# Kernel optimization log

Hardware: AMD Instinct MI355X
Metric: run time of the kernel (lower is better)

The kernel has to match this reference:

```python
import jax, jax.numpy as jnp
import numpy as np

NUM_USERS = 1_000_000
EMBED_DIM = 64
N_NODES = 16384
K = 50
NEG_INF = -1e30


def setup_inputs() -> dict:
    key = jax.random.key(0)
    ks = jax.random.split(key, 7)
    d = EMBED_DIM
    table = jax.random.normal(ks[0], (NUM_USERS, d), jnp.float32) * 0.02
    nodes = jax.random.randint(ks[1], (N_NODES,), 0, NUM_USERS)
    neigh_idx = jax.random.randint(ks[2], (N_NODES, K), 0, NUM_USERS)
    neigh_mask = jax.random.randint(ks[3], (N_NODES, K), 0, 2).astype(bool)
    neigh_mask = neigh_mask.at[:, 0].set(True)  # every node has >=1 neighbor
    W1 = jax.random.normal(ks[4], (2 * d, d), jnp.float32) / np.sqrt(2 * d)
    b1 = jnp.zeros((d,), jnp.float32)
    W2 = jax.random.normal(ks[5], (d, d), jnp.float32) / np.sqrt(d)
    b2 = jnp.zeros((d,), jnp.float32)
    W3 = jax.random.normal(ks[6], (d, 1), jnp.float32) / np.sqrt(d)
    b3 = jnp.zeros((1,), jnp.float32)
    return dict(table=table, W1=W1, b1=b1, W2=W2, b2=b2, W3=W3, b3=b3,
                nodes=nodes, neigh_idx=neigh_idx, neigh_mask=neigh_mask)


def reference(table, W1, b1, W2, b2, W3, b3, nodes, neigh_idx, neigh_mask):
    # Gather neighbor embeddings and center-node embeddings (eval mode: dropout off).
    E = table[neigh_idx]                                   # [N, K, d]
    U = table[nodes]                                       # [N, d]
    Uk = jnp.broadcast_to(U[:, None, :], E.shape)          # [N, K, d]
    x = jnp.concatenate([E, Uk], axis=-1)                  # [N, K, 2d]
    h = jax.nn.relu(x @ W1 + b1)                           # [N, K, d]
    h = jax.nn.relu(h @ W2 + b2)                           # [N, K, d]
    s = (h @ W3 + b3)[..., 0]                              # [N, K]
    # Masked softmax over the ragged neighbor dimension.
    s = jnp.where(neigh_mask, s, NEG_INF)
    att = jax.nn.softmax(s, axis=-1)                       # [N, K]
    # Attention-weighted sum of neighbor embeddings: e_u.T @ att_w per node.
    out = jnp.einsum('nk,nkd->nd', att, E)                 # [N, d]
    return out
```

## Files before the change

### kernel.cpp

```cpp
#include <hip/hip_runtime.h>
#include <hip/hip_bf16.h>

#define NN 16384
#define KK 50
#define DD 64

typedef __attribute__((ext_vector_type(8))) short bf16x8;
typedef __attribute__((ext_vector_type(4))) float f32x4;

__device__ __forceinline__ float bf2f(unsigned short u) {
    union { unsigned int i; float f; } v;
    v.i = ((unsigned int)u) << 16;
    return v.f;
}
__device__ __forceinline__ unsigned short f2bf(float f) {
    union { float f; unsigned int i; } v; v.f = f;
    unsigned int lsb = (v.i >> 16) & 1u;
    v.i += 0x7fffu + lsb;
    return (unsigned short)(v.i >> 16);
}
__device__ __forceinline__ unsigned int pk2bf(float lo, float hi) {
    unsigned int w;
    asm("v_cvt_pk_bf16_f32 %0, %1, %2" : "=v"(w) : "v"(lo), "v"(hi));
    return w;
}

template<int BF16>
__device__ __forceinline__ float ldv(const void* p, size_t i) {
    if (BF16) return bf2f(((const unsigned short*)p)[i]);
    else      return ((const float*)p)[i];
}

template<int BF16>
__device__ __forceinline__ f32x4 ld4(const void* p, size_t i) {
    if (BF16) {
        const ushort4 u = *(const ushort4*)((const unsigned short*)p + i);
        return (f32x4){bf2f(u.x), bf2f(u.y), bf2f(u.z), bf2f(u.w)};
    } else {
        return *(const f32x4*)((const float*)p + i);
    }
}

template<int BF16>
__device__ __forceinline__ bf16x8 load8(const void* p, size_t off) {
    if (BF16) {
        return *(const bf16x8*)((const unsigned short*)p + off);
    } else {
        const float* f = (const float*)p + off;
        const f32x4 a = *(const f32x4*)f;
        const f32x4 b = *(const f32x4*)(f + 4);
        union { bf16x8 v; unsigned int w[4]; } r;
        r.w[0] = pk2bf(a[0], a[1]);
        r.w[1] = pk2bf(a[2], a[3]);
        r.w[2] = pk2bf(b[0], b[1]);
        r.w[3] = pk2bf(b[2], b[3]);
        return r.v;
    }
}

__global__ void prep_kernel(const unsigned int* __restrict__ tw,
                            const unsigned int* __restrict__ mw,
                            const void* __restrict__ W1_,
                            const void* __restrict__ W2_,
                            int* __restrict__ flags,
                            unsigned short* __restrict__ W1top,
                            unsigned short* __restrict__ W1bot,
                            unsigned short* __restrict__ W2p) {
    __shared__ int sflags[2];
    const int t = threadIdx.x;
    if (t < 64) {
        const unsigned int w  = tw[t];
        const unsigned int lo = w & 0xFFFFu;
        const unsigned int ex = (lo >> 7) & 0xFFu;
        const bool bf_like = (ex >= 96u && ex <= 126u);
        const unsigned long long bb = __ballot(bf_like);
        bool found = false;
#pragma unroll
        for (int i = 0; i < 8; ++i) found |= (mw[t + i * 64] > 1u);
        const unsigned long long mb = __ballot(found);
        if (t == 0) {
            sflags[0] = (mb != 0ull) ? 1 : 0;
            sflags[1] = (__popcll(bb) >= 48) ? 1 : 0;
            flags[0] = sflags[0];
            flags[1] = sflags[1];
        }
    }
    __syncthreads();
    const int bf = sflags[1];
    {
        const int f = t >> 6, lane = t & 63;
        const int kt = f >> 2, nt = f & 3;
        const int q = lane >> 4, col = lane & 15;
#pragma unroll
        for (int j = 0; j < 8; ++j) {
            const int k = kt * 32 + q * 8 + j;
            const int n = nt * 16 + col;
            const float v = bf ? bf2f(((const unsigned short*)W1_)[k * 64 + n])
                               : ((const float*)W1_)[k * 64 + n];
            unsigned short* dst = (kt < 2) ? W1top : W1bot;
            const int fl = ((kt & 1) * 4 + nt);
            dst[((size_t)fl * 64 + lane) * 8 + j] = f2bf(v);
        }
    }
    if (t < 512) {
        const int f = t >> 6, lane = t & 63;
        const int kt = f >> 2, nt = f & 3;
        const int q = lane >> 4, col = lane & 15;
#pragma unroll
        for (int j = 0; j < 8; ++j) {
            const int k = kt * 32 + q * 8 + j;
            const int n = nt * 16 + col;
            const float v = bf ? bf2f(((const unsigned short*)W2_)[k * 64 + n])
                               : ((const float*)W2_)[k * 64 + n];
            W2p[((size_t)f * 64 + lane) * 8 + j] = f2bf(v);
        }
    }
}

template<int BF16>
__device__ __forceinline__ void uw_impl(
    const void* __restrict__ table_, const void* __restrict__ b1_,
    const int* __restrict__ nodes,
    const unsigned short* __restrict__ W1bot,
    float* __restrict__ UW)
{
    const int wave = threadIdx.x >> 6;
    const int lane = threadIdx.x & 63;
    const int q    = lane >> 4;
    const int col  = lane & 15;
    const int base = (blockIdx.x * 4 + wave) * 64;

    bf16x8 afrag[4][2];
#pragma unroll
    for (int mt = 0; mt < 4; ++mt) {
        const size_t row = (size_t)nodes[base + mt * 16 + col];
#pragma unroll
        for (int kt = 0; kt < 2; ++kt)
            afrag[mt][kt] = load8<BF16>(table_, row * 64 + kt * 32 + q * 8);
    }

    f32x4 acc[4][4];
#pragma unroll
    for (int mt = 0; mt < 4; ++mt)
#pragma unroll
        for (int nt = 0; nt < 4; ++nt) acc[mt][nt] = (f32x4){0.f, 0.f, 0.f, 0.f};

#pragma unroll
    for (int kt = 0; kt < 2; ++kt)
#pragma unroll
        for (int nt = 0; nt < 4; ++nt) {
            const bf16x8 b = *(const bf16x8*)(W1bot + ((size_t)(kt * 4 + nt) * 64 + lane) * 8);
#pragma unroll
            for (int mt = 0; mt < 4; ++mt)
                acc[mt][nt] = __builtin_amdgcn_mfma_f32_16x16x32_bf16(afrag[mt][kt], b, acc[mt][nt], 0, 0, 0);
        }

    float b1v[4];
#pragma unroll
    for (int nt = 0; nt < 4; ++nt) b1v[nt] = ldv<BF16>(b1_, nt * 16 + col);
#pragma unroll
    for (int mt = 0; mt < 4; ++mt)
#pragma unroll
        for (int nt = 0; nt < 4; ++nt)
#pragma unroll
            for (int r = 0; r < 4; ++r)
                UW[(size_t)(base + mt * 16 + q * 4 + r) * 64 + nt * 16 + col] =
                    acc[mt][nt][r] + b1v[nt];
}

__global__ __launch_bounds__(256) void uw_kernel(
    const void* __restrict__ table_, const void* __restrict__ b1_,
    const int* __restrict__ nodes, const int* __restrict__ flags,
    const unsigned short* __restrict__ W1bot, float* __restrict__ UW)
{
    if (flags[1]) uw_impl<1>(table_, b1_, nodes, W1bot, UW);
    else          uw_impl<0>(table_, b1_, nodes, W1bot, UW);
}

template<int BF16>
__device__ __forceinline__ void agg_impl(
    const void* __restrict__ table_,
    const void* __restrict__ b2_, const void* __restrict__ W3_,
    const int*  __restrict__ neigh_idx,
    const void* __restrict__ neigh_mask,
    int mu8,
    const unsigned short* __restrict__ W1top,
    const unsigned short* __restrict__ W2p,
    const float* __restrict__ UW,
    unsigned short* __restrict__ h1,
    float* __restrict__ scr,
    void* __restrict__ out_)
{
    const int lane = threadIdx.x & 63;
    const int n    = blockIdx.x * 2 + (threadIdx.x >> 6);
    const int q    = lane >> 4;
    const int col  = lane & 15;

    int  rowidx [4];
    bool rowmask[4];
#pragma unroll
    for (int mt = 0; mt < 4; ++mt) {
        const int k  = mt * 16 + col;
        const int kc = (k < KK) ? k : (KK - 1);
        const int ir = neigh_idx[(size_t)n * KK + kc];
        bool mk = mu8 ? (((const unsigned char*)neigh_mask)[(size_t)n * KK + kc] != 0)
                      : (((const int*)neigh_mask)[(size_t)n * KK + kc] != 0);
        mk = mk && (k < KK);
        rowmask[mt] = mk;
        rowidx[mt]  = mk ? ir : 0;
    }

    bf16x8 afrag[4][2];
#pragma unroll
    for (int mt = 0; mt < 4; ++mt)
#pragma unroll
        for (int kt = 0; kt < 2; ++kt)
            afrag[mt][kt] = load8<BF16>(table_, (size_t)rowidx[mt] * 64 + kt * 32 + q * 8);

#pragma unroll
    for (int ct = 0; ct < 4; ++ct) {
        const bf16x8 wA0 = *(const bf16x8*)(W1top + ((size_t)(0 * 4 + ct) * 64 + lane) * 8);
        const bf16x8 wA1 = *(const bf16x8*)(W1top + ((size_t)(1 * 4 + ct) * 64 + lane) * 8);
        f32x4 acc[4];
#pragma unroll
        for (int mt = 0; mt < 4; ++mt) acc[mt] = (f32x4){0.f, 0.f, 0.f, 0.f};
#pragma unroll
        for (int mt = 0; mt < 4; ++mt)
            acc[mt] = __builtin_amdgcn_mfma_f32_16x16x32_bf16(wA0, afrag[mt][0], acc[mt], 0, 0, 0);
#pragma unroll
        for (int mt = 0; mt < 4; ++mt)
            acc[mt] = __builtin_amdgcn_mfma_f32_16x16x32_bf16(wA1, afrag[mt][1], acc[mt], 0, 0, 0);

        const f32x4 uw4 = *(const f32x4*)&UW[(size_t)n * 64 + ct * 16 + q * 4];
#pragma unroll
        for (int mt = 0; mt < 4; ++mt) {
            const float h0 = fmaxf(acc[mt][0] + uw4[0], 0.f);
            const float hv1 = fmaxf(acc[mt][1] + uw4[1], 0.f);
            const float h2 = fmaxf(acc[mt][2] + uw4[2], 0.f);
            const float h3 = fmaxf(acc[mt][3] + uw4[3], 0.f);
            uint2 w;
            w.x = pk2bf(h0, hv1);
            w.y = pk2bf(h2, h3);
            *(uint2*)&h1[(size_t)(mt * 16 + col) * 72 + ct * 16 + q * 4] = w;
        }
    }
    __builtin_amdgcn_wave_barrier();

    bf16x8 bfrag[4][2];
#pragma unroll
    for (int mt = 0; mt < 4; ++mt)
#pragma unroll
        for (int kt = 0; kt < 2; ++kt)
            bfrag[mt][kt] = *(const bf16x8*)&h1[(size_t)(mt * 16 + col) * 72 + kt * 32 + q * 8];

    float p[4] = {0.f, 0.f, 0.f, 0.f};
#pragma unroll
    for (int ct = 0; ct < 4; ++ct) {
        const bf16x8 wB0 = *(const bf16x8*)(W2p + ((size_t)(0 * 4 + ct) * 64 + lane) * 8);
        const bf16x8 wB1 = *(const bf16x8*)(W2p + ((size_t)(1 * 4 + ct) * 64 + lane) * 8);
        f32x4 acc[4];
#pragma unroll
        for (int mt = 0; mt < 4; ++mt) acc[mt] = (f32x4){0.f, 0.f, 0.f, 0.f};
#pragma unroll
        for (int mt = 0; mt < 4; ++mt)
            acc[mt] = __builtin_amdgcn_mfma_f32_16x16x32_bf16(wB0, bfrag[mt][0], acc[mt], 0, 0, 0);
#pragma unroll
        for (int mt = 0; mt < 4; ++mt)
            acc[mt] = __builtin_amdgcn_mfma_f32_16x16x32_bf16(wB1, bfrag[mt][1], acc[mt], 0, 0, 0);

        const f32x4 b2v = ld4<BF16>(b2_, ct * 16 + q * 4);
        const f32x4 w3v = ld4<BF16>(W3_, ct * 16 + q * 4);
#pragma unroll
        for (int mt = 0; mt < 4; ++mt) {
            float t = 0.f;
#pragma unroll
            for (int r = 0; r < 4; ++r)
                t += fmaxf(acc[mt][r] + b2v[r], 0.f) * w3v[r];
            p[mt] += t;
        }
    }

#pragma unroll
    for (int mt = 0; mt < 4; ++mt) {
        p[mt] += __shfl_xor(p[mt], 16, 64);
        p[mt] += __shfl_xor(p[mt], 32, 64);
        if (!rowmask[mt]) p[mt] = -1.0e30f;
    }

    float mx = fmaxf(fmaxf(p[0], p[1]), fmaxf(p[2], p[3]));
    mx = fmaxf(mx, __shfl_xor(mx, 1, 64));
    mx = fmaxf(mx, __shfl_xor(mx, 2, 64));
    mx = fmaxf(mx, __shfl_xor(mx, 4, 64));
    mx = fmaxf(mx, __shfl_xor(mx, 8, 64));

    float e[4], ls = 0.f;
#pragma unroll
    for (int mt = 0; mt < 4; ++mt) { e[mt] = __expf(p[mt] - mx); ls += e[mt]; }
    ls += __shfl_xor(ls, 1, 64);
    ls += __shfl_xor(ls, 2, 64);
    ls += __shfl_xor(ls, 4, 64);
    ls += __shfl_xor(ls, 8, 64);
    const float inv = 1.f / ls;

    float att[4];
#pragma unroll
    for (int mt = 0; mt < 4; ++mt) att[mt] = e[mt] * inv;

    float v[2][8];
#pragma unroll
    for (int kt = 0; kt < 2; ++kt)
#pragma unroll
        for (int j = 0; j < 8; ++j) v[kt][j] = 0.f;
#pragma unroll
    for (int mt = 0; mt < 4; ++mt)
#pragma unroll
        for (int kt = 0; kt < 2; ++kt)
#pragma unroll
            for (int j = 0; j < 8; ++j)
                v[kt][j] += att[mt] * bf2f(((const unsigned short*)&afrag[mt][kt])[j]);

#pragma unroll
    for (int off = 1; off <= 8; off <<= 1)
#pragma unroll
        for (int kt = 0; kt < 2; ++kt)
#pragma unroll
            for (int j = 0; j < 8; ++j)
                v[kt][j] += __shfl_xor(v[kt][j], off, 64);

    if (col == 0) {
#pragma unroll
        for (int kt = 0; kt < 2; ++kt) {
            *(f32x4*)&scr[kt * 32 + q * 8]     = (f32x4){v[kt][0], v[kt][1], v[kt][2], v[kt][3]};
            *(f32x4*)&scr[kt * 32 + q * 8 + 4] = (f32x4){v[kt][4], v[kt][5], v[kt][6], v[kt][7]};
        }
    }
    __builtin_amdgcn_wave_barrier();

    const float res = scr[lane];
    if (BF16) ((unsigned short*)out_)[(size_t)n * 64 + lane] = f2bf(res);
    else      ((float*)out_)[(size_t)n * 64 + lane] = res;
}

__global__ __launch_bounds__(128, 4) void agg_kernel(
    const void* __restrict__ table_,
    const void* __restrict__ b2_, const void* __restrict__ W3_,
    const int*  __restrict__ neigh_idx,
    const void* __restrict__ neigh_mask,
    const int*  __restrict__ flags,
    const unsigned short* __restrict__ W1top,
    const unsigned short* __restrict__ W2p,
    const float* __restrict__ UW,
    void* __restrict__ out_)
{
    __shared__ unsigned short h1_sh[2][64][72];
    __shared__ float scr_sh[2][64];
    const int wave = threadIdx.x >> 6;
    if (flags[1])
        agg_impl<1>(table_, b2_, W3_, neigh_idx, neigh_mask, flags[0],
                    W1top, W2p, UW, &h1_sh[wave][0][0], &scr_sh[wave][0], out_);
    else
        agg_impl<0>(table_, b2_, W3_, neigh_idx, neigh_mask, flags[0],
                    W1top, W2p, UW, &h1_sh[wave][0][0], &scr_sh[wave][0], out_);
}

extern "C" void kernel_launch(void* const* d_in, const int* in_sizes, int n_in,
                              void* d_out, int out_size, void* d_ws, size_t ws_size,
                              hipStream_t stream) {
    const void* table = d_in[0];
    const void* W1    = d_in[1];
    const void* b1    = d_in[2];
    const void* W2    = d_in[3];
    const void* b2    = d_in[4];
    const void* W3    = d_in[5];
    const void* b3    = d_in[6]; (void)b3;
    const int*  nodes = (const int*)d_in[7];
    const int*  nidx  = (const int*)d_in[8];
    const void* nmask = d_in[9];

    char* ws = (char*)d_ws;
    int* flags            = (int*)ws;
    unsigned short* W1top = (unsigned short*)(ws + 1024);
    unsigned short* W1bot = (unsigned short*)(ws + 1024 + 8192);
    unsigned short* W2p   = (unsigned short*)(ws + 1024 + 16384);
    float* UW             = (float*)(ws + 32768);

    prep_kernel<<<1, 1024, 0, stream>>>((const unsigned int*)table,
                                        (const unsigned int*)nmask,
                                        W1, W2, flags, W1top, W1bot, W2p);
    uw_kernel<<<NN / 256, 256, 0, stream>>>(table, b1, nodes, flags, W1bot, UW);
    agg_kernel<<<NN / 2, 128, 0, stream>>>(table, b2, W3, nidx, nmask,
                                           flags, W1top, W2p, UW, d_out);
}
```

Before: 379.2 us.

## Fuse center-node projection into aggregation kernel and reduce via LDS transpose

Removes the separate uw_kernel and its UW round-trip through global memory. Each wave now loads its own center-node row and computes U·W1bot with two extra MFMAs per column tile, adding b1 inline. The final cross-lane reduction of the weighted neighbor sum switches from 4-step shuffles to an LDS transpose reusing the h1 buffer, followed by per-lane summation. Blocks grow to 4 waves (256 threads), which means more LDS per block; the projection MFMA only uses one of 16 useful columns, so some compute is wasted.

```diff
diff --git a/kernel.cpp b/kernel.cpp
--- a/kernel.cpp
+++ b/kernel.cpp
@@ -118,81 +118,22 @@
 }
 
 template<int BF16>
-__device__ __forceinline__ void uw_impl(
-    const void* __restrict__ table_, const void* __restrict__ b1_,
-    const int* __restrict__ nodes,
-    const unsigned short* __restrict__ W1bot,
-    float* __restrict__ UW)
-{
-    const int wave = threadIdx.x >> 6;
-    const int lane = threadIdx.x & 63;
-    const int q    = lane >> 4;
-    const int col  = lane & 15;
-    const int base = (blockIdx.x * 4 + wave) * 64;
-
-    bf16x8 afrag[4][2];
-#pragma unroll
-    for (int mt = 0; mt < 4; ++mt) {
-        const size_t row = (size_t)nodes[base + mt * 16 + col];
-#pragma unroll
-        for (int kt = 0; kt < 2; ++kt)
-            afrag[mt][kt] = load8<BF16>(table_, row * 64 + kt * 32 + q * 8);
-    }
-
-    f32x4 acc[4][4];
-#pragma unroll
-    for (int mt = 0; mt < 4; ++mt)
-#pragma unroll
-        for (int nt = 0; nt < 4; ++nt) acc[mt][nt] = (f32x4){0.f, 0.f, 0.f, 0.f};
-
-#pragma unroll
-    for (int kt = 0; kt < 2; ++kt)
-#pragma unroll
-        for (int nt = 0; nt < 4; ++nt) {
-            const bf16x8 b = *(const bf16x8*)(W1bot + ((size_t)(kt * 4 + nt) * 64 + lane) * 8);
-#pragma unroll
-            for (int mt = 0; mt < 4; ++mt)
-                acc[mt][nt] = __builtin_amdgcn_mfma_f32_16x16x32_bf16(afrag[mt][kt], b, acc[mt][nt], 0, 0, 0);
-        }
-
-    float b1v[4];
-#pragma unroll
-    for (int nt = 0; nt < 4; ++nt) b1v[nt] = ldv<BF16>(b1_, nt * 16 + col);
-#pragma unroll
-    for (int mt = 0; mt < 4; ++mt)
-#pragma unroll
-        for (int nt = 0; nt < 4; ++nt)
-#pragma unroll
-            for (int r = 0; r < 4; ++r)
-                UW[(size_t)(base + mt * 16 + q * 4 + r) * 64 + nt * 16 + col] =
-                    acc[mt][nt][r] + b1v[nt];
-}
-
-__global__ __launch_bounds__(256) void uw_kernel(
-    const void* __restrict__ table_, const void* __restrict__ b1_,
-    const int* __restrict__ nodes, const int* __restrict__ flags,
-    const unsigned short* __restrict__ W1bot, float* __restrict__ UW)
-{
-    if (flags[1]) uw_impl<1>(table_, b1_, nodes, W1bot, UW);
-    else          uw_impl<0>(table_, b1_, nodes, W1bot, UW);
-}
-
-template<int BF16>
 __device__ __forceinline__ void agg_impl(
     const void* __restrict__ table_,
+    const void* __restrict__ b1_,
     const void* __restrict__ b2_, const void* __restrict__ W3_,
+    const int*  __restrict__ nodes,
     const int*  __restrict__ neigh_idx,
     const void* __restrict__ neigh_mask,
     int mu8,
     const unsigned short* __restrict__ W1top,
+    const unsigned short* __restrict__ W1bot,
     const unsigned short* __restrict__ W2p,
-    const float* __restrict__ UW,
     unsigned short* __restrict__ h1,
-    float* __restrict__ scr,
     void* __restrict__ out_)
 {
     const int lane = threadIdx.x & 63;
-    const int n    = blockIdx.x * 2 + (threadIdx.x >> 6);
+    const int n    = blockIdx.x * 4 + (threadIdx.x >> 6);
     const int q    = lane >> 4;
     const int col  = lane & 15;
 
@@ -210,6 +151,12 @@
         rowidx[mt]  = mk ? ir : 0;
     }
 
+    const size_t urow = (size_t)nodes[n];
+    bf16x8 ufrag[2];
+#pragma unroll
+    for (int kt = 0; kt < 2; ++kt)
+        ufrag[kt] = load8<BF16>(table_, urow * 64 + kt * 32 + q * 8);
+
     bf16x8 afrag[4][2];
 #pragma unroll
     for (int mt = 0; mt < 4; ++mt)
@@ -221,23 +168,32 @@
     for (int ct = 0; ct < 4; ++ct) {
         const bf16x8 wA0 = *(const bf16x8*)(W1top + ((size_t)(0 * 4 + ct) * 64 + lane) * 8);
         const bf16x8 wA1 = *(const bf16x8*)(W1top + ((size_t)(1 * 4 + ct) * 64 + lane) * 8);
+        const bf16x8 uB0 = *(const bf16x8*)(W1bot + ((size_t)(0 * 4 + ct) * 64 + lane) * 8);
+        const bf16x8 uB1 = *(const bf16x8*)(W1bot + ((size_t)(1 * 4 + ct) * 64 + lane) * 8);
         f32x4 acc[4];
 #pragma unroll
         for (int mt = 0; mt < 4; ++mt) acc[mt] = (f32x4){0.f, 0.f, 0.f, 0.f};
+        f32x4 accu = (f32x4){0.f, 0.f, 0.f, 0.f};
 #pragma unroll
         for (int mt = 0; mt < 4; ++mt)
             acc[mt] = __builtin_amdgcn_mfma_f32_16x16x32_bf16(wA0, afrag[mt][0], acc[mt], 0, 0, 0);
+        accu = __builtin_amdgcn_mfma_f32_16x16x32_bf16(uB0, ufrag[0], accu, 0, 0, 0);
 #pragma unroll
         for (int mt = 0; mt < 4; ++mt)
             acc[mt] = __builtin_amdgcn_mfma_f32_16x16x32_bf16(wA1, afrag[mt][1], acc[mt], 0, 0, 0);
-
-        const f32x4 uw4 = *(const f32x4*)&UW[(size_t)n * 64 + ct * 16 + q * 4];
+        accu = __builtin_amdgcn_mfma_f32_16x16x32_bf16(uB1, ufrag[1], accu, 0, 0, 0);
+
+        const f32x4 b1v = ld4<BF16>(b1_, ct * 16 + q * 4);
+        const float uw0 = accu[0] + b1v[0];
+        const float uw1 = accu[1] + b1v[1];
+        const float uw2 = accu[2] + b1v[2];
+        const float uw3 = accu[3] + b1v[3];
 #pragma unroll
         for (int mt = 0; mt < 4; ++mt) {
-            const float h0 = fmaxf(acc[mt][0] + uw4[0], 0.f);
-            const float hv1 = fmaxf(acc[mt][1] + uw4[1], 0.f);
-            const float h2 = fmaxf(acc[mt][2] + uw4[2], 0.f);
-            const float h3 = fmaxf(acc[mt][3] + uw4[3], 0.f);
+            const float h0 = fmaxf(acc[mt][0] + uw0, 0.f);
+            const float hv1 = fmaxf(acc[mt][1] + uw1, 0.f);
+            const float h2 = fmaxf(acc[mt][2] + uw2, 0.f);
+            const float h3 = fmaxf(acc[mt][3] + uw3, 0.f);
             uint2 w;
             w.x = pk2bf(h0, hv1);
             w.y = pk2bf(h2, h3);
@@ -319,48 +275,49 @@
             for (int j = 0; j < 8; ++j)
                 v[kt][j] += att[mt] * bf2f(((const unsigned short*)&afrag[mt][kt])[j]);
 
-#pragma unroll
-    for (int off = 1; off <= 8; off <<= 1)
-#pragma unroll
-        for (int kt = 0; kt < 2; ++kt)
-#pragma unroll
-            for (int j = 0; j < 8; ++j)
-                v[kt][j] += __shfl_xor(v[kt][j], off, 64);
-
-    if (col == 0) {
-#pragma unroll
-        for (int kt = 0; kt < 2; ++kt) {
-            *(f32x4*)&scr[kt * 32 + q * 8]     = (f32x4){v[kt][0], v[kt][1], v[kt][2], v[kt][3]};
-            *(f32x4*)&scr[kt * 32 + q * 8 + 4] = (f32x4){v[kt][4], v[kt][5], v[kt][6], v[kt][7]};
-        }
-    }
+    float* part = (float*)h1;
     __builtin_amdgcn_wave_barrier();
-
-    const float res = scr[lane];
+#pragma unroll
+    for (int kt = 0; kt < 2; ++kt)
+#pragma unroll
+        for (int j = 0; j < 8; ++j)
+            part[(kt * 32 + q * 8 + j) * 20 + col] = v[kt][j];
+    __builtin_amdgcn_wave_barrier();
+
+    const f32x4 s0 = *(const f32x4*)&part[lane * 20 + 0];
+    const f32x4 s1 = *(const f32x4*)&part[lane * 20 + 4];
+    const f32x4 s2 = *(const f32x4*)&part[lane * 20 + 8];
+    const f32x4 s3 = *(const f32x4*)&part[lane * 20 + 12];
+    const float res = (((s0[0] + s0[1]) + (s0[2] + s0[3]))
+                     + ((s1[0] + s1[1]) + (s1[2] + s1[3])))
+                    + (((s2[0] + s2[1]) + (s2[2] + s2[3]))
+                     + ((s3[0] + s3[1]) + (s3[2] + s3[3])));
+
     if (BF16) ((unsigned short*)out_)[(size_t)n * 64 + lane] = f2bf(res);
     else      ((float*)out_)[(size_t)n * 64 + lane] = res;
 }
 
-__global__ __launch_bounds__(128, 4) void agg_kernel(
+__global__ __launch_bounds__(256, 4) void agg_kernel(
     const void* __restrict__ table_,
+    const void* __restrict__ b1_,
     const void* __restrict__ b2_, const void* __restrict__ W3_,
+    const int*  __restrict__ nodes,
     const int*  __restrict__ neigh_idx,
     const void* __restrict__ neigh_mask,
     const int*  __restrict__ flags,
     const unsigned short* __restrict__ W1top,
+    const unsigned short* __restrict__ W1bot,
     const unsigned short* __restrict__ W2p,
-    const float* __restrict__ UW,
     void* __restrict__ out_)
 {
-    __shared__ unsigned short h1_sh[2][64][72];
-    __shared__ float scr_sh[2][64];
+    __shared__ unsigned short h1_sh[4][64][72];
     const int wave = threadIdx.x >> 6;
     if (flags[1])
-        agg_impl<1>(table_, b2_, W3_, neigh_idx, neigh_mask, flags[0],
-                    W1top, W2p, UW, &h1_sh[wave][0][0], &scr_sh[wave][0], out_);
+        agg_impl<1>(table_, b1_, b2_, W3_, nodes, neigh_idx, neigh_mask, flags[0],
+                    W1top, W1bot, W2p, &h1_sh[wave][0][0], out_);
     else
-        agg_impl<0>(table_, b2_, W3_, neigh_idx, neigh_mask, flags[0],
-                    W1top, W2p, UW, &h1_sh[wave][0][0], &scr_sh[wave][0], out_);
+        agg_impl<0>(table_, b1_, b2_, W3_, nodes, neigh_idx, neigh_mask, flags[0],
+                    W1top, W1bot, W2p, &h1_sh[wave][0][0], out_);
 }
 
 extern "C" void kernel_launch(void* const* d_in, const int* in_sizes, int n_in,
@@ -382,12 +339,10 @@
     unsigned short* W1top = (unsigned short*)(ws + 1024);
     unsigned short* W1bot = (unsigned short*)(ws + 1024 + 8192);
     unsigned short* W2p   = (unsigned short*)(ws + 1024 + 16384);
-    float* UW             = (float*)(ws + 32768);
 
     prep_kernel<<<1, 1024, 0, stream>>>((const unsigned int*)table,
                                         (const unsigned int*)nmask,
                                         W1, W2, flags, W1top, W1bot, W2p);
-    uw_kernel<<<NN / 256, 256, 0, stream>>>(table, b1, nodes, flags, W1bot, UW);
-    agg_kernel<<<NN / 2, 128, 0, stream>>>(table, b2, W3, nidx, nmask,
-                                           flags, W1top, W2p, UW, d_out);
-}
+    agg_kernel<<<NN / 4, 256, 0, stream>>>(table, b1, b2, W3, nodes, nidx, nmask,
+                                           flags, W1top, W1bot, W2p, d_out);
+}
```

Result: faster. 367.0 us (-3.2%).
